# Kernel tuning notes

Measured on AMD Instinct MI355X. Metric: run time of the kernel, lower is better.

The kernel has to match this reference:

```python
import jax, jax.numpy as jnp
import numpy as np

HASHCODE_LEN = 8   # config.attention_hashcode_len (tau)
NUM_HEAD = 12      # config.num_attention_heads
KERNEL = 9         # config.attention_conv_kernel_size
B, H, S, D = 2, 12, 2048, 64


def _l2_normalize(x, eps=1e-12):
    # yoso.normalize: L2-normalize along last (head_dim) axis
    return x / jnp.maximum(jnp.linalg.norm(x, axis=-1, keepdims=True), eps)


def setup_inputs() -> dict:
    key = jax.random.key(0)
    kq, kk, kv, kw = jax.random.split(key, 4)
    Q = jax.random.normal(kq, (B, H, S, D), jnp.float32)
    K = jax.random.normal(kk, (B, H, S, D), jnp.float32)
    V = jax.random.normal(kv, (B, H, S, D), jnp.float32)
    mask = jnp.ones((B, S), jnp.float32)
    conv_w = jax.random.normal(kw, (H, 1, KERNEL, 1), jnp.float32) * 0.02
    return {"Q": Q, "K": K, "V": V, "mask": mask, "conv_w": conv_w}


def reference(Q, K, V, mask, conv_w):
    # conv skip path: depthwise (groups=num_head) Conv2d over the seq axis of masked V
    Vm = V * mask[:, None, :, None]                       # [B,H,S,D]
    conv_V = jax.lax.conv_general_dilated(
        Vm, conv_w, window_strides=(1, 1),
        padding=((KERNEL // 2, KERNEL // 2), (0, 0)),
        dimension_numbers=("NCHW", "OIHW", "NCHW"),
        feature_group_count=H)

    # yoso_e exact-expectation branch (num_hash_f < 0): normalize Q, K, then
    # attention weight = E[hash collision] = (1 - arccos(q.k)/pi)^hashcode_len
    Qn = _l2_normalize(Q)
    Kn = _l2_normalize(K)
    qk = jnp.einsum("bhsd,bhtd->bhst", Qn, Kn)            # [B,H,S,S]
    qk = jnp.clip(qk, -1.0 + 1e-6, 1.0 - 1e-6)            # keep arccos grad finite
    w = (1.0 - jnp.arccos(qk) / jnp.pi) ** HASHCODE_LEN
    w = w * mask[:, None, None, :]                        # key-side mask
    X = jnp.einsum("bhst,bhtd->bhsd", w, V)
    X = X * mask[:, None, :, None]                        # query-side mask
    X = _l2_normalize(X)                                  # yoso.normalize(X)
    return X + conv_V
```

## Files before the change

### kernel.cpp

```cpp
#include <hip/hip_runtime.h>
#include <hip/hip_bf16.h>
#include <math.h>

typedef __attribute__((ext_vector_type(4)))  float f32x4;
typedef __attribute__((ext_vector_type(16))) float f32x16;
typedef __attribute__((ext_vector_type(8)))  short bf16x8;
typedef __attribute__((ext_vector_type(4)))  int   i32x4;

#define NB 2
#define NH 12
#define NS 2048
#define ND 64
#define NKER 9
#define BH (NB*NH)
#define BHS (NB*NH*NS)
#define TK 128
#define NT (NS/TK)

using bf16 = __hip_bfloat16;

__device__ __forceinline__ f32x16 mfma32(bf16x8 a, bf16x8 b, f32x16 c) {
  return __builtin_amdgcn_mfma_f32_32x32x16_bf16(a, b, c, 0, 0, 0);
}

__device__ __forceinline__ unsigned short bf16rne(float f) {
  unsigned u = __builtin_bit_cast(unsigned, f);
  u += 0x7FFFu + ((u >> 16) & 1u);
  return (unsigned short)(u >> 16);
}

__device__ __forceinline__ int cvtpk_bf16(float lo, float hi) {
  int d;
  asm("v_cvt_pk_bf16_f32 %0, %1, %2" : "=v"(d) : "v"(lo), "v"(hi));
  return d;
}

__global__ __launch_bounds__(256) void prep(
    const float* __restrict__ K, const float* __restrict__ V,
    const float* __restrict__ mask, const float* __restrict__ cw,
    float* __restrict__ out, bf16* __restrict__ Kn, bf16* __restrict__ Vmt) {
  __shared__ float tile[72][68];
  __shared__ float wsm[NKER];
  int bh = blockIdx.y, b = bh / NH, h = bh % NH;
  int s0 = blockIdx.x * 64;
  int tid = threadIdx.x;
  if (tid < NKER) wsm[tid] = cw[h * NKER + tid];

  int r  = tid >> 2;
  int c0 = (tid & 3) * 16;

  {
    const float* Kr = K + ((size_t)bh * NS + s0 + r) * ND + c0;
    float v[16]; float ss = 0.f;
    #pragma unroll
    for (int j = 0; j < 16; ++j) { v[j] = Kr[j]; ss += v[j] * v[j]; }
    ss += __shfl_xor(ss, 1); ss += __shfl_xor(ss, 2);
    float sc = rsqrtf(fmaxf(ss, 1e-24f));
    bf16x8 o0, o1;
    #pragma unroll
    for (int j = 0; j < 8; ++j) {
      o0[j] = (short)bf16rne(v[j] * sc);
      o1[j] = (short)bf16rne(v[8 + j] * sc);
    }
    bf16* dst = Kn + ((size_t)bh * NS + s0 + r) * ND + c0;
    *(bf16x8*)dst = o0; *(bf16x8*)(dst + 8) = o1;
  }

  #pragma unroll
  for (int pass = 0; pass < 2; ++pass) {
    int rr = r + pass * 64;
    if (pass == 0 || tid < 32) {
      int gs = s0 - NKER / 2 + rr;
      bool ok = (gs >= 0 && gs < NS);
      float m = ok ? mask[b * NS + gs] : 0.f;
      #pragma unroll
      for (int j = 0; j < 16; ++j)
        tile[rr][c0 + j] = ok ? V[((size_t)bh * NS + gs) * ND + c0 + j] * m : 0.f;
    }
  }
  __syncthreads();

  {
    float acc[16];
    #pragma unroll
    for (int j = 0; j < 16; ++j) acc[j] = 0.f;
    #pragma unroll
    for (int k = 0; k < NKER; ++k) {
      float w = wsm[k];
      #pragma unroll
      for (int j = 0; j < 16; ++j) acc[j] += tile[r + k][c0 + j] * w;
    }
    float* dst = out + ((size_t)bh * NS + s0 + r) * ND + c0;
    #pragma unroll
    for (int j = 0; j < 16; ++j) dst[j] = acc[j];
  }
  {
    bf16x8 o0, o1;
    #pragma unroll
    for (int j = 0; j < 8; ++j) {
      o0[j] = (short)bf16rne(tile[NKER / 2 + c0 + j][r]);
      o1[j] = (short)bf16rne(tile[NKER / 2 + c0 + 8 + j][r]);
    }
    bf16* dst = Vmt + (size_t)bh * ND * NS + (size_t)r * NS + s0 + c0;
    *(bf16x8*)dst = o0; *(bf16x8*)(dst + 8) = o1;
  }
}

__global__ __launch_bounds__(512) void yoso_attn(
    const float* __restrict__ Q, const bf16* __restrict__ Kn,
    const bf16* __restrict__ Vmt, const float* __restrict__ mask,
    float* __restrict__ out) {
  __shared__ __align__(16) char lds[48 * 1024];

  int tid  = threadIdx.x;
  int wave = tid >> 6;
  int lane = tid & 63;
  int ql   = lane & 31;
  int c    = lane >> 5;
  int qsub = wave >> 2;
  int kh   = wave & 3;

  int bx  = blockIdx.x;
  int idx = bx >> 3;
  int bh  = (bx & 7) + 8 * (idx >> 5);
  int qg  = idx & 31;
  int b   = bh / NH;
  int q0  = qg * 64;

  const bf16* Kbh = Kn  + (size_t)bh * NS * ND;
  const bf16* Vbh = Vmt + (size_t)bh * ND * NS;

  bf16x8 aq[4];
  {
    int qrow = q0 + qsub * 32 + ql;
    const float* Qr = Q + ((size_t)bh * NS + qrow) * ND;
    float qv[32]; float ss = 0.f;
    #pragma unroll
    for (int t = 0; t < 4; ++t) {
      f32x4 a0 = *(const f32x4*)(Qr + t * 16 + c * 8);
      f32x4 a1 = *(const f32x4*)(Qr + t * 16 + c * 8 + 4);
      #pragma unroll
      for (int j = 0; j < 4; ++j) {
        qv[t * 8 + j] = a0[j]; qv[t * 8 + 4 + j] = a1[j];
        ss += a0[j] * a0[j] + a1[j] * a1[j];
      }
    }
    ss += __shfl_xor(ss, 32);
    float sc = rsqrtf(fmaxf(ss, 1e-24f));
    #pragma unroll
    for (int t = 0; t < 4; ++t)
      #pragma unroll
      for (int j = 0; j < 8; ++j)
        aq[t][j] = (short)bf16rne(qv[t * 8 + j] * sc);
  }

  f32x16 xa0{}, xa1{};

  int kr0r = tid >> 3,          kr0c = (tid & 7) * 16;
  int kr1r = (tid + 512) >> 3,  kr1c = kr0c;
  int vr0r = tid >> 4,          vr0c = (tid & 15) * 16;
  int vr1r = (tid + 512) >> 4,  vr1c = vr0c;
  int kd0 = kr0r * 128 + (kr0c ^ ((kr0r & 7) << 4));
  int kd1 = kr1r * 128 + (kr1c ^ ((kr1r & 7) << 4));
  int vd0 = 16384 + vr0r * 256 + (vr0c ^ ((vr0r & 7) << 4));
  int vd1 = 16384 + vr1r * 256 + (vr1c ^ ((vr1r & 7) << 4));
  const char* KsA = (const char*)Kbh + (size_t)kr0r * 128 + kr0c;
  const char* KsB = (const char*)Kbh + (size_t)kr1r * 128 + kr1c;
  const char* VsA = (const char*)Vbh + (size_t)vr0r * (NS * 2) + vr0c;
  const char* VsB = (const char*)Vbh + (size_t)vr1r * (NS * 2) + vr1c;

  *(i32x4*)(lds + kd0) = *(const i32x4*)KsA;
  *(i32x4*)(lds + kd1) = *(const i32x4*)KsB;
  *(i32x4*)(lds + vd0) = *(const i32x4*)VsA;
  *(i32x4*)(lds + vd1) = *(const i32x4*)VsB;

  int krow = kh * 32 + ql;
  int ksw  = (krow & 7) << 4;
  int kboff[4];
  #pragma unroll
  for (int t = 0; t < 4; ++t) kboff[t] = krow * 128 + ((t * 32 + c * 16) ^ ksw);
  int bvoff[2][2];
  #pragma unroll
  for (int dt = 0; dt < 2; ++dt) {
    int drow = dt * 32 + ql;
    int vsw  = (drow & 7) << 4;
    #pragma unroll
    for (int ks = 0; ks < 2; ++ks)
      bvoff[dt][ks] = 16384 + drow * 256 + ((kh * 64 + ks * 32 + c * 16) ^ vsw);
  }

  i32x4 kA, kB, vA, vB;

  for (int kt = 0; kt < NT; ++kt) {
    __syncthreads();
    if (kt < NT - 1) {
      kA = *(const i32x4*)(KsA + (size_t)(kt + 1) * 16384);
      kB = *(const i32x4*)(KsB + (size_t)(kt + 1) * 16384);
      vA = *(const i32x4*)(VsA + (size_t)(kt + 1) * 256);
      vB = *(const i32x4*)(VsB + (size_t)(kt + 1) * 256);
    }

    bf16x8 ak0 = *(const bf16x8*)(lds + kboff[0]);
    bf16x8 ak1 = *(const bf16x8*)(lds + kboff[1]);
    bf16x8 ak2 = *(const bf16x8*)(lds + kboff[2]);
    bf16x8 ak3 = *(const bf16x8*)(lds + kboff[3]);
    f32x16 s{};
    s = mfma32(ak0, aq[0], s);
    s = mfma32(ak1, aq[1], s);
    s = mfma32(ak2, aq[2], s);
    s = mfma32(ak3, aq[3], s);

    int pk[8];
    #pragma unroll
    for (int g = 0; g < 4; ++g) {
      float wq[4];
      #pragma unroll
      for (int j = 0; j < 4; ++j) {
        float x = s[g * 4 + j];
        float a = fminf(fabsf(x), 0.999999f);
        float sq = __builtin_amdgcn_sqrtf(1.0f - a);
        float p = fmaf(fmaf(fmaf(-0.005961377f, a, 0.02363857f), a,
                            -0.06751758f), a, 0.49998939f);
        float u = sq * p;
        float t1 = (x >= 0.0f) ? (1.0f - u) : u;
        float t2 = t1 * t1, t4 = t2 * t2;
        wq[j] = t4 * t4;
      }
      pk[g * 2]     = cvtpk_bf16(wq[0], wq[1]);
      pk[g * 2 + 1] = cvtpk_bf16(wq[2], wq[3]);
    }
    int xpk[8];
    #pragma unroll
    for (int i = 0; i < 8; ++i) xpk[i] = __shfl_xor(pk[i], 32);
    i32x4 pa0i = c ? (i32x4){xpk[2], xpk[3], pk[2], pk[3]}
                   : (i32x4){pk[0], pk[1], xpk[0], xpk[1]};
    i32x4 pa1i = c ? (i32x4){xpk[6], xpk[7], pk[6], pk[7]}
                   : (i32x4){pk[4], pk[5], xpk[4], xpk[5]};
    bf16x8 pa0 = __builtin_bit_cast(bf16x8, pa0i);
    bf16x8 pa1 = __builtin_bit_cast(bf16x8, pa1i);

    bf16x8 bv00 = *(const bf16x8*)(lds + bvoff[0][0]);
    bf16x8 bv10 = *(const bf16x8*)(lds + bvoff[1][0]);
    bf16x8 bv01 = *(const bf16x8*)(lds + bvoff[0][1]);
    bf16x8 bv11 = *(const bf16x8*)(lds + bvoff[1][1]);
    xa0 = mfma32(pa0, bv00, xa0);
    xa1 = mfma32(pa0, bv10, xa1);
    xa0 = mfma32(pa1, bv01, xa0);
    xa1 = mfma32(pa1, bv11, xa1);

    __syncthreads();
    if (kt < NT - 1) {
      *(i32x4*)(lds + kd0) = kA;
      *(i32x4*)(lds + kd1) = kB;
      *(i32x4*)(lds + vd0) = vA;
      *(i32x4*)(lds + vd1) = vB;
    }
  }

  float (*cmb)[64][64] = (float(*)[64][64])lds;
  if (kh != 0) {
    #pragma unroll
    for (int r = 0; r < 16; ++r) {
      int qrow = qsub * 32 + (r & 3) + 8 * (r >> 2) + 4 * c;
      cmb[kh - 1][qrow][ql]      = xa0[r];
      cmb[kh - 1][qrow][32 + ql] = xa1[r];
    }
  }
  __syncthreads();
  if (kh == 0) {
    #pragma unroll
    for (int r = 0; r < 16; ++r) {
      int qloc = (r & 3) + 8 * (r >> 2) + 4 * c;
      int qrow = qsub * 32 + qloc;
      int row  = q0 + qrow;
      float m  = mask[b * NS + row];
      float x0 = (xa0[r] + cmb[0][qrow][ql] + cmb[1][qrow][ql] + cmb[2][qrow][ql]) * m;
      float x1 = (xa1[r] + cmb[0][qrow][32 + ql] + cmb[1][qrow][32 + ql] + cmb[2][qrow][32 + ql]) * m;
      float s2 = x0 * x0 + x1 * x1;
      #pragma unroll
      for (int mm = 1; mm < 32; mm <<= 1) s2 += __shfl_xor(s2, mm);
      float sc = rsqrtf(fmaxf(s2, 1e-24f));
      size_t base = ((size_t)bh * NS + row) * ND;
      out[base + ql]      += x0 * sc;
      out[base + 32 + ql] += x1 * sc;
    }
  }
}

extern "C" void kernel_launch(void* const* d_in, const int* in_sizes, int n_in,
                              void* d_out, int out_size, void* d_ws, size_t ws_size,
                              hipStream_t stream) {
  const float* Q    = (const float*)d_in[0];
  const float* K    = (const float*)d_in[1];
  const float* V    = (const float*)d_in[2];
  const float* mask = (const float*)d_in[3];
  const float* cw   = (const float*)d_in[4];
  float* out = (float*)d_out;

  bf16* Kn  = (bf16*)d_ws;
  bf16* Vmt = Kn + (size_t)BHS * ND;

  prep<<<dim3(NS / 64, BH), 256, 0, stream>>>(K, V, mask, cw, out, Kn, Vmt);
  yoso_attn<<<(NS / 64) * BH, 512, 0, stream>>>(Q, Kn, Vmt, mask, out);
}
```

Before: 89.65 us.

## Use direct global-to-LDS loads and a branchless arccos polynomial

Result: slower. 93.44 us (+4.2%).

```diff
diff --git a/kernel.cpp b/kernel.cpp
--- a/kernel.cpp
+++ b/kernel.cpp
@@ -34,6 +34,11 @@
   asm("v_cvt_pk_bf16_f32 %0, %1, %2" : "=v"(d) : "v"(lo), "v"(hi));
   return d;
 }
+
+#define GLDS(gsrc, ldst)                                                     \
+  __builtin_amdgcn_global_load_lds(                                          \
+      (const __attribute__((address_space(1))) void*)(gsrc),                 \
+      (__attribute__((address_space(3))) void*)(ldst), 16, 0, 0)
 
 __global__ __launch_bounds__(256) void prep(
     const float* __restrict__ K, const float* __restrict__ V,
@@ -106,7 +111,7 @@
   }
 }
 
-__global__ __launch_bounds__(512) void yoso_attn(
+__global__ __launch_bounds__(512, 6) void yoso_attn(
     const float* __restrict__ Q, const bf16* __restrict__ Kn,
     const bf16* __restrict__ Vmt, const float* __restrict__ mask,
     float* __restrict__ out) {
@@ -156,23 +161,24 @@
 
   f32x16 xa0{}, xa1{};
 
-  int kr0r = tid >> 3,          kr0c = (tid & 7) * 16;
-  int kr1r = (tid + 512) >> 3,  kr1c = kr0c;
-  int vr0r = tid >> 4,          vr0c = (tid & 15) * 16;
-  int vr1r = (tid + 512) >> 4,  vr1c = vr0c;
-  int kd0 = kr0r * 128 + (kr0c ^ ((kr0r & 7) << 4));
-  int kd1 = kr1r * 128 + (kr1c ^ ((kr1r & 7) << 4));
-  int vd0 = 16384 + vr0r * 256 + (vr0c ^ ((vr0r & 7) << 4));
-  int vd1 = 16384 + vr1r * 256 + (vr1c ^ ((vr1r & 7) << 4));
-  const char* KsA = (const char*)Kbh + (size_t)kr0r * 128 + kr0c;
-  const char* KsB = (const char*)Kbh + (size_t)kr1r * 128 + kr1c;
-  const char* VsA = (const char*)Vbh + (size_t)vr0r * (NS * 2) + vr0c;
-  const char* VsB = (const char*)Vbh + (size_t)vr1r * (NS * 2) + vr1c;
-
-  *(i32x4*)(lds + kd0) = *(const i32x4*)KsA;
-  *(i32x4*)(lds + kd1) = *(const i32x4*)KsB;
-  *(i32x4*)(lds + vd0) = *(const i32x4*)VsA;
-  *(i32x4*)(lds + vd1) = *(const i32x4*)VsB;
+  int c0i = tid, c1i = tid + 512;
+  int k0row = c0i >> 3, k1row = c1i >> 3;
+  int v0row = c0i >> 4, v1row = c1i >> 4;
+  const char* Ksrc0 = (const char*)Kbh + (size_t)k0row * 128 +
+                      (((c0i & 7) * 16) ^ ((k0row & 7) << 4));
+  const char* Ksrc1 = (const char*)Kbh + (size_t)k1row * 128 +
+                      (((c1i & 7) * 16) ^ ((k1row & 7) << 4));
+  const char* Vsrc0 = (const char*)Vbh + (size_t)v0row * (NS * 2) +
+                      (((c0i & 15) * 16) ^ ((v0row & 7) << 4));
+  const char* Vsrc1 = (const char*)Vbh + (size_t)v1row * (NS * 2) +
+                      (((c1i & 15) * 16) ^ ((v1row & 7) << 4));
+  char* ldsK = lds + wave * 1024;
+  char* ldsV = lds + 16384 + wave * 1024;
+
+  GLDS(Ksrc0, ldsK);
+  GLDS(Ksrc1, ldsK + 8192);
+  GLDS(Vsrc0, ldsV);
+  GLDS(Vsrc1, ldsV + 8192);
 
   int krow = kh * 32 + ql;
   int ksw  = (krow & 7) << 4;
@@ -189,16 +195,8 @@
       bvoff[dt][ks] = 16384 + drow * 256 + ((kh * 64 + ks * 32 + c * 16) ^ vsw);
   }
 
-  i32x4 kA, kB, vA, vB;
-
   for (int kt = 0; kt < NT; ++kt) {
     __syncthreads();
-    if (kt < NT - 1) {
-      kA = *(const i32x4*)(KsA + (size_t)(kt + 1) * 16384);
-      kB = *(const i32x4*)(KsB + (size_t)(kt + 1) * 16384);
-      vA = *(const i32x4*)(VsA + (size_t)(kt + 1) * 256);
-      vB = *(const i32x4*)(VsB + (size_t)(kt + 1) * 256);
-    }
 
     bf16x8 ak0 = *(const bf16x8*)(lds + kboff[0]);
     bf16x8 ak1 = *(const bf16x8*)(lds + kboff[1]);
@@ -216,13 +214,13 @@
       float wq[4];
       #pragma unroll
       for (int j = 0; j < 4; ++j) {
-        float x = s[g * 4 + j];
-        float a = fminf(fabsf(x), 0.999999f);
-        float sq = __builtin_amdgcn_sqrtf(1.0f - a);
-        float p = fmaf(fmaf(fmaf(-0.005961377f, a, 0.02363857f), a,
-                            -0.06751758f), a, 0.49998939f);
-        float u = sq * p;
-        float t1 = (x >= 0.0f) ? (1.0f - u) : u;
+        float x  = fminf(s[g * 4 + j], 0.999999f);
+        float u  = 1.0f - x;
+        float sq = __builtin_amdgcn_sqrtf(u);
+        float gg = fmaf(fmaf(fmaf(fmaf(8.54787e-4f, u, 2.512043e-3f), u,
+                                  8.440465e-3f), u, 3.7513178e-2f), u,
+                        0.45015816f);
+        float t1 = fmaf(-sq, gg, 1.0f);
         float t2 = t1 * t1, t4 = t2 * t2;
         wq[j] = t4 * t4;
       }
@@ -250,10 +248,10 @@
 
     __syncthreads();
     if (kt < NT - 1) {
-      *(i32x4*)(lds + kd0) = kA;
-      *(i32x4*)(lds + kd1) = kB;
-      *(i32x4*)(lds + vd0) = vA;
-      *(i32x4*)(lds + vd1) = vB;
+      GLDS(Ksrc0 + (size_t)(kt + 1) * 16384, ldsK);
+      GLDS(Ksrc1 + (size_t)(kt + 1) * 16384, ldsK + 8192);
+      GLDS(Vsrc0 + (size_t)(kt + 1) * 256,  ldsV);
+      GLDS(Vsrc1 + (size_t)(kt + 1) * 256,  ldsV + 8192);
     }
   }
 
```
